# Performance work log

Measured on AMD Instinct MI355X. Metric: run time of the kernel, lower is better.

The kernel has to match this reference:

```python
import jax, jax.numpy as jnp
import numpy as np

ROT_DEG = 15.0
TRANS_FRAC = 0.1
B, C, H, W = 64, 3, 384, 384


def setup_inputs() -> dict:
    key = jax.random.key(0)
    k1, k2, k3, k4 = jax.random.split(key, 4)
    x = jax.random.uniform(k1, (B, C, H, W), dtype=jnp.float32)
    # per-sample random affine params, mirroring torch.rand()*2-1 scaling
    angles = (jax.random.uniform(k2, (B,), dtype=jnp.float32) * 2 - 1) * ROT_DEG
    dx = (jax.random.uniform(k3, (B,), dtype=jnp.float32) * 2 - 1) * (TRANS_FRAC * W)
    dy = (jax.random.uniform(k4, (B,), dtype=jnp.float32) * 2 - 1) * (TRANS_FRAC * H)
    return {"x": x, "angles": angles, "dx": dx, "dy": dy}


def _affine_sample_one(img, angle_deg, tx, ty):
    # img: (C,H,W). Rotation about image center + pixel translation,
    # bilinear sampling, zeros fill outside (mode='black').
    c_, h, w = img.shape
    cx = (w - 1) * 0.5
    cy = (h - 1) * 0.5
    yo, xo = jnp.meshgrid(
        jnp.arange(h, dtype=img.dtype) - cy,
        jnp.arange(w, dtype=img.dtype) - cx,
        indexing="ij",
    )  # centered output pixel coords, each (H,W)
    rad = angle_deg * (jnp.pi / 180.0)
    co = jnp.cos(rad)
    si = jnp.sin(rad)
    # inverse affine: output pixel -> input source coord (torchvision convention)
    xs = co * (xo - tx) + si * (yo - ty) + cx
    ys = -si * (xo - tx) + co * (yo - ty) + cy
    x0 = jnp.floor(xs)
    y0 = jnp.floor(ys)
    wx = xs - x0
    wy = ys - y0
    x0i = x0.astype(jnp.int32)
    y0i = y0.astype(jnp.int32)

    def gather(yi, xi):
        valid = (xi >= 0) & (xi < w) & (yi >= 0) & (yi < h)
        xc = jnp.clip(xi, 0, w - 1)
        yc = jnp.clip(yi, 0, h - 1)
        v = img[:, yc, xc]  # (C,H,W)
        return v * valid.astype(img.dtype)

    v00 = gather(y0i, x0i)
    v01 = gather(y0i, x0i + 1)
    v10 = gather(y0i + 1, x0i)
    v11 = gather(y0i + 1, x0i + 1)
    return (
        v00 * (1 - wx) * (1 - wy)
        + v01 * wx * (1 - wy)
        + v10 * (1 - wx) * wy
        + v11 * wx * wy
    )


def reference(x, angles, dx, dy):
    y = jax.vmap(_affine_sample_one)(x, angles, dx, dy)
    return jnp.clip(y, 0.0, 1.0)
```

## Files before the change

### kernel.cpp

```cpp
#include <hip/hip_runtime.h>
#include <hip/hip_bf16.h>
#include <math.h>

#define BB 64
#define CC 3
#define HH 384
#define WW 384
#define HW (HH * WW)

#define TILE_W 64
#define TILE_H 16
#define TX_TILES (WW / TILE_W)
#define TY_TILES (HH / TILE_H)
#define TILES_PER_IMG (TX_TILES * TY_TILES)
#define NBLOCKS (BB * TILES_PER_IMG)

#define LW_STRIDE 71
#define LH_MAX 36

__global__ __launch_bounds__(512, 8) void GeometricAugment_kernel(
    const float* __restrict__ x,
    const float* __restrict__ angles,
    const float* __restrict__ dx,
    const float* __restrict__ dy,
    float* __restrict__ out) {

    __shared__ float lds[CC * LH_MAX * LW_STRIDE];

    int bid = blockIdx.x;
    int swz = (bid & 7) * (NBLOCKS / 8) + (bid >> 3);

    int b   = swz / TILES_PER_IMG;
    int t   = swz - b * TILES_PER_IMG;
    int tyb = t / TX_TILES;
    int txb = t - tyb * TX_TILES;

    int tid = threadIdx.x;
    int tx  = tid & 63;
    int tyl = tid >> 6;

    const int X0 = txb * TILE_W;
    const int Y0 = tyb * TILE_H;

    const float cx = (WW - 1) * 0.5f;
    const float cy = (HH - 1) * 0.5f;

    float rad = angles[b] * (float)(M_PI / 180.0);
    float si, co;
    __sincosf(rad, &si, &co);
    float txs = dx[b];
    float tys = dy[b];

    float xo0 = (float)X0 - cx - txs;
    float xo1 = (float)(X0 + TILE_W - 1) - cx - txs;
    float yo0 = (float)Y0 - cy - tys;
    float yo1 = (float)(Y0 + TILE_H - 1) - cy - tys;

    float xsA = co * xo0 + si * yo0 + cx;
    float xsB = co * xo1 + si * yo0 + cx;
    float xsC = co * xo0 + si * yo1 + cx;
    float xsD = co * xo1 + si * yo1 + cx;
    float ysA = -si * xo0 + co * yo0 + cy;
    float ysB = -si * xo1 + co * yo0 + cy;
    float ysC = -si * xo0 + co * yo1 + cy;
    float ysD = -si * xo1 + co * yo1 + cy;

    float xsmin = fminf(fminf(xsA, xsB), fminf(xsC, xsD));
    float xsmax = fmaxf(fmaxf(xsA, xsB), fmaxf(xsC, xsD));
    float ysmin = fminf(fminf(ysA, ysB), fminf(ysC, ysD));
    float ysmax = fmaxf(fmaxf(ysA, ysB), fmaxf(ysC, ysD));

    int ximin = (int)floorf(xsmin) - 1;
    int yimin = (int)floorf(ysmin) - 1;
    int LH = (int)floorf(ysmax) + 2 - yimin + 1;
    LH = min(LH, LH_MAX);

    const float* imgb = x + (size_t)b * CC * HW;

    int nelem = LH * LW_STRIDE;
    for (int i = tid; i < nelem; i += 512) {
        int y  = i / LW_STRIDE;
        int xL = i - y * LW_STRIDE;
        int gy = min(max(yimin + y, 0), HH - 1);
        int gx = min(max(ximin + xL, 0), WW - 1);
        const float* src = imgb + gy * WW + gx;
        #pragma unroll
        for (int c = 0; c < CC; ++c) {
            lds[c * (LH_MAX * LW_STRIDE) + i] = src[c * HW];
        }
    }
    __syncthreads();

    int x_out = X0 + tx;
    float xo = (float)x_out - cx - txs;

    float* outb = out + (size_t)b * CC * HW + (size_t)Y0 * WW + x_out;

    #pragma unroll
    for (int r = 0; r < TILE_H / 8; ++r) {
        int yrow = tyl + r * 8;
        float yo = (float)(Y0 + yrow) - cy - tys;

        float xs =  co * xo + si * yo + cx;
        float ys = -si * xo + co * yo + cy;

        float x0f = floorf(xs);
        float y0f = floorf(ys);
        float wx = xs - x0f;
        float wy = ys - y0f;
        int x0 = (int)x0f;
        int y0 = (int)y0f;
        int x1 = x0 + 1;
        int y1 = y0 + 1;

        float vx0 = (x0 >= 0 && x0 < WW) ? 1.0f : 0.0f;
        float vx1 = (x1 >= 0 && x1 < WW) ? 1.0f : 0.0f;
        float vy0 = (y0 >= 0 && y0 < HH) ? 1.0f : 0.0f;
        float vy1 = (y1 >= 0 && y1 < HH) ? 1.0f : 0.0f;

        float w00 = (1.0f - wx) * (1.0f - wy) * vx0 * vy0;
        float w01 = wx * (1.0f - wy) * vx1 * vy0;
        float w10 = (1.0f - wx) * wy * vx0 * vy1;
        float w11 = wx * wy * vx1 * vy1;

        int xL0 = x0 - ximin;
        int yL0 = y0 - yimin;

        int base = yL0 * LW_STRIDE + xL0;

        #pragma unroll
        for (int c = 0; c < CC; ++c) {
            const float* l = lds + c * (LH_MAX * LW_STRIDE) + base;
            float v00 = l[0];
            float v01 = l[1];
            float v10 = l[LW_STRIDE];
            float v11 = l[LW_STRIDE + 1];
            float v = v00 * w00 + v01 * w01 + v10 * w10 + v11 * w11;
            v = fminf(fmaxf(v, 0.0f), 1.0f);
            __builtin_nontemporal_store(v, outb + (size_t)c * HW + (size_t)yrow * WW);
        }
    }
}

extern "C" void kernel_launch(void* const* d_in, const int* in_sizes, int n_in,
                              void* d_out, int out_size, void* d_ws, size_t ws_size,
                              hipStream_t stream) {
    const float* x      = (const float*)d_in[0];
    const float* angles = (const float*)d_in[1];
    const float* dx     = (const float*)d_in[2];
    const float* dy     = (const float*)d_in[3];
    float* out = (float*)d_out;

    GeometricAugment_kernel<<<NBLOCKS, 512, 0, stream>>>(x, angles, dx, dy, out);
}
```

Measured before the change: 42.13 us.

## Enlarge row tile and add fast interior path skipping bounds checks

```diff
diff --git a/kernel.cpp b/kernel.cpp
--- a/kernel.cpp
+++ b/kernel.cpp
@@ -9,14 +9,15 @@
 #define HW (HH * WW)
 
 #define TILE_W 64
-#define TILE_H 16
+#define TILE_H 24
 #define TX_TILES (WW / TILE_W)
 #define TY_TILES (HH / TILE_H)
 #define TILES_PER_IMG (TX_TILES * TY_TILES)
 #define NBLOCKS (BB * TILES_PER_IMG)
 
 #define LW_STRIDE 71
-#define LH_MAX 36
+#define LH_MAX 43
+#define LCH (LH_MAX * LW_STRIDE)
 
 __global__ __launch_bounds__(512, 8) void GeometricAugment_kernel(
     const float* __restrict__ x,
@@ -25,7 +26,7 @@
     const float* __restrict__ dy,
     float* __restrict__ out) {
 
-    __shared__ float lds[CC * LH_MAX * LW_STRIDE];
+    __shared__ float lds[CC * LCH];
 
     int bid = blockIdx.x;
     int swz = (bid & 7) * (NBLOCKS / 8) + (bid >> 3);
@@ -75,69 +76,109 @@
     int LH = (int)floorf(ysmax) + 2 - yimin + 1;
     LH = min(LH, LH_MAX);
 
+    bool interior = (ximin >= 0) && (yimin >= 0) &&
+                    (ximin + LW_STRIDE <= WW) && (yimin + LH <= HH);
+
     const float* imgb = x + (size_t)b * CC * HW;
 
     int nelem = LH * LW_STRIDE;
-    for (int i = tid; i < nelem; i += 512) {
-        int y  = i / LW_STRIDE;
-        int xL = i - y * LW_STRIDE;
-        int gy = min(max(yimin + y, 0), HH - 1);
-        int gx = min(max(ximin + xL, 0), WW - 1);
-        const float* src = imgb + gy * WW + gx;
-        #pragma unroll
-        for (int c = 0; c < CC; ++c) {
-            lds[c * (LH_MAX * LW_STRIDE) + i] = src[c * HW];
+    if (interior) {
+        const float* srcb = imgb + yimin * WW + ximin;
+        for (int i = tid; i < nelem; i += 512) {
+            int y  = i / LW_STRIDE;
+            int xL = i - y * LW_STRIDE;
+            const float* src = srcb + y * WW + xL;
+            #pragma unroll
+            for (int c = 0; c < CC; ++c)
+                lds[c * LCH + i] = src[c * HW];
+        }
+    } else {
+        for (int i = tid; i < nelem; i += 512) {
+            int y  = i / LW_STRIDE;
+            int xL = i - y * LW_STRIDE;
+            int gy = min(max(yimin + y, 0), HH - 1);
+            int gx = min(max(ximin + xL, 0), WW - 1);
+            const float* src = imgb + gy * WW + gx;
+            #pragma unroll
+            for (int c = 0; c < CC; ++c)
+                lds[c * LCH + i] = src[c * HW];
         }
     }
     __syncthreads();
 
     int x_out = X0 + tx;
     float xo = (float)x_out - cx - txs;
+    float yo = (float)(Y0 + tyl) - cy - tys;
+
+    float xs =  co * xo + si * yo + cx;
+    float ys = -si * xo + co * yo + cy;
+    const float dxs = 8.0f * si;
+    const float dys = 8.0f * co;
 
     float* outb = out + (size_t)b * CC * HW + (size_t)Y0 * WW + x_out;
 
-    #pragma unroll
-    for (int r = 0; r < TILE_H / 8; ++r) {
-        int yrow = tyl + r * 8;
-        float yo = (float)(Y0 + yrow) - cy - tys;
+    if (interior) {
+        #pragma unroll
+        for (int r = 0; r < TILE_H / 8; ++r) {
+            float x0f = floorf(xs);
+            float y0f = floorf(ys);
+            float wx = xs - x0f;
+            float wy = ys - y0f;
+            int base = ((int)y0f - yimin) * LW_STRIDE + ((int)x0f - ximin);
 
-        float xs =  co * xo + si * yo + cx;
-        float ys = -si * xo + co * yo + cy;
+            #pragma unroll
+            for (int c = 0; c < CC; ++c) {
+                const float* l = lds + c * LCH + base;
+                float v00 = l[0];
+                float v01 = l[1];
+                float v10 = l[LW_STRIDE];
+                float v11 = l[LW_STRIDE + 1];
+                float top = v00 + wx * (v01 - v00);
+                float bot = v10 + wx * (v11 - v10);
+                float v = top + wy * (bot - top);
+                v = fminf(fmaxf(v, 0.0f), 1.0f);
+                __builtin_nontemporal_store(v, outb + (size_t)c * HW + (size_t)(tyl + r * 8) * WW);
+            }
+            xs += dxs;
+            ys += dys;
+        }
+    } else {
+        #pragma unroll
+        for (int r = 0; r < TILE_H / 8; ++r) {
+            float x0f = floorf(xs);
+            float y0f = floorf(ys);
+            float wx = xs - x0f;
+            float wy = ys - y0f;
+            int x0 = (int)x0f;
+            int y0 = (int)y0f;
+            int x1 = x0 + 1;
+            int y1 = y0 + 1;
 
-        float x0f = floorf(xs);
-        float y0f = floorf(ys);
-        float wx = xs - x0f;
-        float wy = ys - y0f;
-        int x0 = (int)x0f;
-        int y0 = (int)y0f;
-        int x1 = x0 + 1;
-        int y1 = y0 + 1;
+            float vx0 = (x0 >= 0 && x0 < WW) ? 1.0f : 0.0f;
+            float vx1 = (x1 >= 0 && x1 < WW) ? 1.0f : 0.0f;
+            float vy0 = (y0 >= 0 && y0 < HH) ? 1.0f : 0.0f;
+            float vy1 = (y1 >= 0 && y1 < HH) ? 1.0f : 0.0f;
 
-        float vx0 = (x0 >= 0 && x0 < WW) ? 1.0f : 0.0f;
-        float vx1 = (x1 >= 0 && x1 < WW) ? 1.0f : 0.0f;
-        float vy0 = (y0 >= 0 && y0 < HH) ? 1.0f : 0.0f;
-        float vy1 = (y1 >= 0 && y1 < HH) ? 1.0f : 0.0f;
+            float w00 = (1.0f - wx) * (1.0f - wy) * vx0 * vy0;
+            float w01 = wx * (1.0f - wy) * vx1 * vy0;
+            float w10 = (1.0f - wx) * wy * vx0 * vy1;
+            float w11 = wx * wy * vx1 * vy1;
 
-        float w00 = (1.0f - wx) * (1.0f - wy) * vx0 * vy0;
-        float w01 = wx * (1.0f - wy) * vx1 * vy0;
-        float w10 = (1.0f - wx) * wy * vx0 * vy1;
-        float w11 = wx * wy * vx1 * vy1;
+            int base = (y0 - yimin) * LW_STRIDE + (x0 - ximin);
 
-        int xL0 = x0 - ximin;
-        int yL0 = y0 - yimin;
-
-        int base = yL0 * LW_STRIDE + xL0;
-
-        #pragma unroll
-        for (int c = 0; c < CC; ++c) {
-            const float* l = lds + c * (LH_MAX * LW_STRIDE) + base;
-            float v00 = l[0];
-            float v01 = l[1];
-            float v10 = l[LW_STRIDE];
-            float v11 = l[LW_STRIDE + 1];
-            float v = v00 * w00 + v01 * w01 + v10 * w10 + v11 * w11;
-            v = fminf(fmaxf(v, 0.0f), 1.0f);
-            __builtin_nontemporal_store(v, outb + (size_t)c * HW + (size_t)yrow * WW);
+            #pragma unroll
+            for (int c = 0; c < CC; ++c) {
+                const float* l = lds + c * LCH + base;
+                float v00 = l[0];
+                float v01 = l[1];
+                float v10 = l[LW_STRIDE];
+                float v11 = l[LW_STRIDE + 1];
+                float v = v00 * w00 + v01 * w01 + v10 * w10 + v11 * w11;
+                v = fminf(fmaxf(v, 0.0f), 1.0f);
+                __builtin_nontemporal_store(v, outb + (size_t)c * HW + (size_t)(tyl + r * 8) * WW);
+            }
+            xs += dxs;
+            ys += dys;
         }
     }
 }
```

Measured after the change: 39.83 us. 1.06x faster.
